# Optimization experiments

Measured on AMD Instinct MI355X. Metric: run time of the kernel, lower is better.

Reference implementation:

```python
import jax, jax.numpy as jnp
import numpy as np
from jax import lax

TEMPLATE = 21          # template_size
SEARCH = 9             # search_range
PAD = TEMPLATE // 2    # conv padding


def setup_inputs() -> dict:
    key = jax.random.key(0)
    k1, k2 = jax.random.split(key)
    B, H, W = 4, 480, 640
    p1 = jax.random.uniform(k1, (B, 1, H, W), dtype=jnp.float32)
    p2 = jax.random.uniform(k2, (B, 1, H, W), dtype=jnp.float32)
    return {"p1": p1, "p2": p2}


def _box_sum(x):
    # 21x21 box filter (conv with all-ones kernel), same padding, stride 1.
    kernel = jnp.ones((1, 1, TEMPLATE, TEMPLATE), x.dtype)
    return lax.conv_general_dilated(x, kernel, (1, 1), [(PAD, PAD), (PAD, PAD)])


def reference(p1, p2):
    p1 = p1.astype(jnp.float32)
    p2 = p2.astype(jnp.float32)
    B, _, H, W = p1.shape
    R = SEARCH

    # zero-pad search margin around p2
    p2_padded = jnp.pad(p2, ((0, 0), (0, 0), (R, R), (R, R)))

    # (361, 2) offsets, iterated dy-major / dx-minor to match the torch loop order
    dys, dxs = jnp.meshgrid(jnp.arange(-R, R + 1), jnp.arange(-R, R + 1), indexing='ij')
    offsets = jnp.stack([dys.reshape(-1), dxs.reshape(-1)], axis=-1)  # rows: (dy, dx)

    max0 = jnp.full((B, 1, H, W), -1.0, dtype=jnp.float32)
    flow0 = jnp.zeros((B, 2, H, W), dtype=jnp.float32)

    def step(carry, off):
        max_score, flow = carry
        dy, dx = off[0], off[1]
        shifted = lax.dynamic_slice(p2_padded, (0, 0, R + dy, R + dx), (B, 1, H, W))
        agreement = p1 * shifted + (1.0 - p1) * (1.0 - shifted)
        corr = _box_sum(agreement)                  # (B,1,H,W)
        mask = corr > max_score
        max_score = jnp.where(mask, corr, max_score)
        m = mask[:, 0]                               # (B,H,W)
        fx = jnp.where(m, dx.astype(jnp.float32), flow[:, 0])
        fy = jnp.where(m, dy.astype(jnp.float32), flow[:, 1])
        flow = jnp.stack([fx, fy], axis=1)
        return (max_score, flow), None

    (max_score, flow), _ = lax.scan(step, (max0, flow0), offsets)

    particle_density = _box_sum(p1)
    confidence = jnp.clip(particle_density / float(TEMPLATE * TEMPLATE), 0.0, 1.0)
    return flow, confidence
```

## Files before the change

### kernel.cpp

```cpp
#include <hip/hip_runtime.h>


#define HH 480
#define WW 640
#define TH 32
#define TW 32
#define QROWS 52
#define PROWS 70
#define PCOLS 70
#define PSTR  71
#define RSTR  36
#define MARGIN 0.002f
#define NPIX (4 * HH * WW)

__device__ __forceinline__ float replay_corr(const float* __restrict__ p1b,
                                             const float* __restrict__ p2b,
                                             int y, int x, int k) {
  int dy = k / 19 - 9, dx = k % 19 - 9;
  float s = 0.f;
  for (int u = 0; u < 21; ++u) {
    int yy = y - 10 + u;
    if (yy < 0 || yy >= HH) continue;
    int y2 = yy + dy;
    bool yok = (y2 >= 0 && y2 < HH);
    const float* r1 = p1b + yy * WW;
    const float* r2 = p2b + y2 * WW;
#pragma unroll
    for (int v = 0; v < 21; ++v) {
      int xx = x - 10 + v;
      if (xx < 0 || xx >= WW) continue;
      float p = r1[xx];
      int x2 = xx + dx;
      float s2 = (yok && x2 >= 0 && x2 < WW) ? r2[x2] : 0.f;
      float t2 = __fmul_rn(__fsub_rn(1.f, p), __fsub_rn(1.f, s2));
      float agr = __fmaf_rn(p, s2, t2);
      s = __fadd_rn(s, agr);
    }
  }
  return s;
}

__global__ __launch_bounds__(256, 4)
void bcm_pass1(const float* __restrict__ p1, const float* __restrict__ p2,
               float* __restrict__ out, unsigned* __restrict__ wl,
               unsigned capE) {
  __shared__ float ps[PROWS * PSTR];
  __shared__ __align__(16) float rsb0[QROWS * RSTR];
  __shared__ __align__(16) float rsb1[QROWS * RSTR];

  const int tid = threadIdx.x;
  const int b  = blockIdx.z;
  const int y0 = blockIdx.y * TH;
  const int x0 = blockIdx.x * TW;
  const float* p1b = p1 + b * HH * WW;
  const float* p2b = p2 + b * HH * WW;

  for (int i = tid; i < PROWS * PCOLS; i += 256) {
    int rr = i / PCOLS, cc = i - rr * PCOLS;
    int Y = y0 - 19 + rr, X = x0 - 19 + cc;
    float v = 0.f;
    if (Y >= 0 && Y < HH && X >= 0 && X < WW) v = p2b[Y * WW + X];
    ps[rr * PSTR + cc] = v;
  }

  const int col = tid & 31;
  const int r0  = (tid >> 5) * 4;
  const int prow_ = tid >> 2;
  const int c0    = (tid & 3) * 8;
  const bool active1 = (prow_ < QROWS);

  float qreg[28];
  if (active1) {
    int Y = y0 - 10 + prow_;
    bool yok = (Y >= 0 && Y < HH);
    const float* qrow = p1b + Y * WW;
#pragma unroll
    for (int t = 0; t < 28; ++t) {
      int X = x0 - 10 + c0 + t;
      float v = 0.f;
      if (yok && X >= 0 && X < WW) v = 2.f * qrow[X] - 1.f;
      qreg[t] = v;
    }
  }
  __syncthreads();

  float bv[4][4];
  int   bk[4][4];
#pragma unroll
  for (int j = 0; j < 4; ++j)
#pragma unroll
    for (int t = 0; t < 4; ++t) { bv[j][t] = -1e30f; bk[j][t] = 0; }

  float preg[28];
  int k = 0;
  for (int dy = -9; dy <= 9; ++dy) {
    const float* prowp = active1 ? &ps[(prow_ + dy + 9) * PSTR + c0] : ps;
    if (active1) {
#pragma unroll
      for (int t = 0; t < 28; ++t) preg[t] = prowp[t];
    }
#pragma unroll
    for (int dxi = 0; dxi < 19; ++dxi, ++k) {
      float* slab = (k & 1) ? rsb1 : rsb0;
      if (active1) {
        float s = 0.f;
#pragma unroll
        for (int t = 0; t < 21; ++t) s += qreg[t] * preg[(dxi + t) % 28];
        float rs[8];
        rs[0] = s;
#pragma unroll
        for (int j = 1; j < 8; ++j) {
          s += qreg[j + 20] * preg[(dxi + j + 20) % 28]
             - qreg[j - 1] * preg[(dxi + j - 1) % 28];
          rs[j] = s;
        }
        float4* w = (float4*)&slab[prow_ * RSTR + c0];
        w[0] = make_float4(rs[0], rs[1], rs[2], rs[3]);
        w[1] = make_float4(rs[4], rs[5], rs[6], rs[7]);
        if (dxi < 18) preg[dxi % 28] = prowp[dxi + 28];
      }
      __syncthreads();
      {
        float s = 0.f;
#pragma unroll
        for (int u = 0; u < 21; ++u) s += slab[(r0 + u) * RSTR + col];
#pragma unroll
        for (int j = 0; j < 4; ++j) {
          if (j > 0) s += slab[(r0 + 20 + j) * RSTR + col]
                        - slab[(r0 + j - 1) * RSTR + col];
          float cv = s;
          if (cv > bv[j][3]) {
            int ck = k;
#pragma unroll
            for (int t = 0; t < 4; ++t) {
              if (cv > bv[j][t]) {
                float tv = bv[j][t]; int tk = bk[j][t];
                bv[j][t] = cv; bk[j][t] = ck;
                cv = tv; ck = tk;
              }
            }
          }
        }
      }
    }
  }

  __syncthreads();
  if (active1) {
    float s = 0.f;
#pragma unroll
    for (int t = 0; t < 21; ++t) s += qreg[t];
    float rs[8];
    rs[0] = s;
#pragma unroll
    for (int j = 1; j < 8; ++j) {
      s += qreg[j + 20] - qreg[j - 1];
      rs[j] = s;
    }
    float4* w = (float4*)&rsb0[prow_ * RSTR + c0];
    w[0] = make_float4(rs[0], rs[1], rs[2], rs[3]);
    w[1] = make_float4(rs[4], rs[5], rs[6], rs[7]);
  }
  __syncthreads();

  unsigned* cntN = wl;
  unsigned* cntD = wl + 1;
  uint4* entries = (uint4*)(wl + 8);
  const unsigned capHalf = capE >> 1;
  const int confoff = 4 * 2 * HH * WW;
  {
    float s = 0.f;
#pragma unroll
    for (int u = 0; u < 21; ++u) s += rsb0[(r0 + u) * RSTR + col];
#pragma unroll
    for (int j = 0; j < 4; ++j) {
      if (j > 0) s += rsb0[(r0 + 20 + j) * RSTR + col]
                    - rsb0[(r0 + j - 1) * RSTR + col];
      int y = y0 + r0 + j;
      int x = x0 + col;
      int ny = min(y + 10, HH - 1) - max(y - 10, 0) + 1;
      int nx = min(x + 10, WW - 1) - max(x - 10, 0) + 1;
      float c = (s + (float)(ny * nx)) * (1.f / 882.f);
      float conf = fminf(fmaxf(c, 0.f), 1.f);

      int kwin = bk[j][0];
      float ofx = (float)(kwin % 19 - 9);
      float ofy = (float)(kwin / 19 - 9);

      if (bv[j][0] - bv[j][1] <= MARGIN) {
        int cand[4];
        int n = 1; cand[0] = bk[j][0];
#pragma unroll
        for (int t = 1; t < 4; ++t)
          if (bv[j][0] - bv[j][t] <= MARGIN) cand[n++] = bk[j][t];
        bool deep = (bv[j][0] - bv[j][3] <= MARGIN);
        unsigned pix = (unsigned)((b * HH + y) * WW + x);
        bool stored = false;
        if (!deep) {
          unsigned slot = atomicAdd(cntN, 1u);
          if (slot < capHalf) {
            unsigned kk[4];
#pragma unroll
            for (int t = 0; t < 4; ++t)
              kk[t] = (t < n) ? (unsigned)cand[t] : 0xFFFFu;
            uint4 e;
            e.x = pix;
            e.y = kk[0] | (kk[1] << 16);
            e.z = kk[2] | (kk[3] << 16);
            e.w = 0u;
            entries[slot] = e;
            stored = true;
          }
        } else {
          unsigned ds = atomicAdd(cntD, 1u);
          if (ds < capHalf) {
            uint4 e; e.x = pix; e.y = 0u; e.z = 0u; e.w = 0u;
            entries[capE - 1 - ds] = e;
            stored = true;
          }
        }
        if (!stored) {
          int c2 = (n > 2) ? cand[2] : cand[0];
          int c3 = (n > 3) ? cand[3] : cand[0];
          int dpf = deep ? 1 : 0;
          ofx = (float)(1000000 + cand[0] + 512 * cand[1]);
          ofy = (float)(c2 + 512 * c3 + 262144 * dpf);
        }
      }
      out[((b * 2 + 0) * HH + y) * WW + x] = ofx;
      out[((b * 2 + 1) * HH + y) * WW + x] = ofy;
      out[confoff + (b * HH + y) * WW + x] = conf;
    }
  }
}

__global__ __launch_bounds__(256)
void bcm_pass2(const float* __restrict__ p1, const float* __restrict__ p2,
               float* __restrict__ out, const unsigned* __restrict__ wl,
               unsigned capE) {
  const unsigned capHalf = capE >> 1;
  unsigned rawN = wl[0], rawD = wl[1];
  unsigned nN = rawN > capHalf ? capHalf : rawN;
  unsigned nD = rawD > capHalf ? capHalf : rawD;
  const uint4* entries = (const uint4*)(wl + 8);
  const int lane = threadIdx.x & 63;
  unsigned wid = blockIdx.x * (blockDim.x >> 6) + (threadIdx.x >> 6);
  unsigned nw = gridDim.x * (blockDim.x >> 6);

  for (unsigned base = wid * 16; base < nN; base += nw * 16) {
    unsigned e = base + (lane >> 2);
    int c = lane & 3;
    float wv = -1e30f;
    int   wk = 0x7FFF;
    unsigned pix = 0;
    bool valid = (e < nN);
    if (valid) {
      uint4 ent = entries[e];
      pix = ent.x;
      unsigned kc = (c == 0) ? (ent.y & 0xFFFFu) :
                    (c == 1) ? (ent.y >> 16) :
                    (c == 2) ? (ent.z & 0xFFFFu) : (ent.z >> 16);
      if (kc != 0xFFFFu) {
        int b = pix / (HH * WW);
        int r = pix - b * (HH * WW);
        int y = r / WW, x = r - y * WW;
        wv = replay_corr(p1 + b * HH * WW, p2 + b * HH * WW, y, x, (int)kc);
        wk = (int)kc;
      }
    }
#pragma unroll
    for (int d = 1; d <= 2; d <<= 1) {
      float ov = __shfl_xor(wv, d, 64);
      int   ok = __shfl_xor(wk, d, 64);
      if (ov > wv || (ov == wv && ok < wk)) { wv = ov; wk = ok; }
    }
    if (valid && c == 0) {
      int b = pix / (HH * WW);
      int r = pix - b * (HH * WW);
      int y = r / WW, x = r - y * WW;
      int fxi = (b * 2 * HH + y) * WW + x;
      out[fxi] = (float)(wk % 19 - 9);
      out[fxi + HH * WW] = (float)(wk / 19 - 9);
    }
  }

  for (unsigned d = wid; d < nD; d += nw) {
    uint4 ent = entries[capE - 1 - d];
    unsigned pix = ent.x;
    int b = pix / (HH * WW);
    int r = pix - b * (HH * WW);
    int y = r / WW, x = r - y * WW;
    const float* p1b = p1 + b * HH * WW;
    const float* p2b = p2 + b * HH * WW;
    float wv = -1e30f;
    int   wk = 0x7FFF;
    for (int k = lane; k < 361; k += 64) {
      float s = replay_corr(p1b, p2b, y, x, k);
      if (s > wv || (s == wv && k < wk)) { wv = s; wk = k; }
    }
    for (int off = 32; off > 0; off >>= 1) {
      float ov = __shfl_down(wv, off, 64);
      int   ok = __shfl_down(wk, off, 64);
      if (ov > wv || (ov == wv && ok < wk)) { wv = ov; wk = ok; }
    }
    if (lane == 0) {
      int fxi = (b * 2 * HH + y) * WW + x;
      out[fxi] = (float)(wk % 19 - 9);
      out[fxi + HH * WW] = (float)(wk / 19 - 9);
    }
  }

  if (rawN > capHalf || rawD > capHalf) {
    int stride = gridDim.x * blockDim.x;
    for (int idx = blockIdx.x * blockDim.x + threadIdx.x; idx < NPIX;
         idx += stride) {
      int b = idx / (HH * WW);
      int r = idx - b * (HH * WW);
      int fxi = b * 2 * HH * WW + r;
      float fx = out[fxi];
      if (fx < 500000.f) continue;
      int fyi = fxi + HH * WW;
      int p = (int)fx - 1000000;
      int q = (int)out[fyi];
      int deep = q >> 18;
      int kk[4] = {p & 511, p >> 9, q & 511, (q >> 9) & 511};
      int y = r / WW, x = r - y * WW;
      const float* p1b = p1 + b * HH * WW;
      const float* p2b = p2 + b * HH * WW;
      float wv = 0.f; int win = -1;
      if (deep) {
        for (int k = 0; k < 361; ++k) {
          float s = replay_corr(p1b, p2b, y, x, k);
          if (win < 0 || s > wv) { wv = s; win = k; }
        }
      } else {
        for (int c = 0; c < 4; ++c) {
          int k = kk[c];
          float s = replay_corr(p1b, p2b, y, x, k);
          if (win < 0 || s > wv || (s == wv && k < win)) { wv = s; win = k; }
        }
      }
      out[fxi] = (float)(win % 19 - 9);
      out[fyi] = (float)(win / 19 - 9);
    }
  }
}

extern "C" void kernel_launch(void* const* d_in, const int* in_sizes, int n_in,
                              void* d_out, int out_size, void* d_ws, size_t ws_size,
                              hipStream_t stream) {
  const float* p1 = (const float*)d_in[0];
  const float* p2 = (const float*)d_in[1];
  float* out = (float*)d_out;
  unsigned* wl = (unsigned*)d_ws;
  unsigned capE = (ws_size >= 64) ? (unsigned)((ws_size - 32) / 16) : 0u;
  hipMemsetAsync(d_ws, 0, 32, stream);
  dim3 grid1(WW / TW, HH / TH, 4);
  bcm_pass1<<<grid1, dim3(256), 0, stream>>>(p1, p2, out, wl, capE);
  bcm_pass2<<<dim3(512), dim3(256), 0, stream>>>(p1, p2, out, wl, capE);
}
```

Baseline: 720.7 us.

## Split FMA reduction chains into independent accumulators and wave-parallelize overflow replay

The row-sum and column-sum reductions in the main correlation loop now use four independent accumulators and precomputed sliding deltas instead of one serial dependency chain, aiming for more instruction-level parallelism. Column loads are hoisted into a register array. The overflow fallback path, which replayed correlations one pixel per thread, now ballots flagged pixels within each wave and replays each one cooperatively across the 64 lanes through a shared helper. Reassociating the float sums can change rounding, which risks flipping near-tie argmax decisions and adds register pressure.

```diff
diff --git a/kernel.cpp b/kernel.cpp
--- a/kernel.cpp
+++ b/kernel.cpp
@@ -40,6 +40,41 @@
   return s;
 }
 
+__device__ __forceinline__ void replay_reduce_write(
+    const float* p1, const float* p2, float* out,
+    unsigned pix, bool deep, unsigned k0, unsigned k1, unsigned k2,
+    unsigned k3, int lane) {
+  int b = pix / (HH * WW);
+  int r = pix - b * (HH * WW);
+  int y = r / WW, x = r - y * WW;
+  const float* p1b = p1 + b * HH * WW;
+  const float* p2b = p2 + b * HH * WW;
+  float wv = -1e30f;
+  int   wk = 0x7FFF;
+  if (deep) {
+    for (int k = lane; k < 361; k += 64) {
+      float s = replay_corr(p1b, p2b, y, x, k);
+      if (s > wv || (s == wv && k < wk)) { wv = s; wk = k; }
+    }
+  } else if (lane < 4) {
+    unsigned kc = (lane == 0) ? k0 : (lane == 1) ? k1 : (lane == 2) ? k2 : k3;
+    if (kc != 0xFFFFu) {
+      wv = replay_corr(p1b, p2b, y, x, (int)kc);
+      wk = (int)kc;
+    }
+  }
+  for (int off = 32; off > 0; off >>= 1) {
+    float ov = __shfl_down(wv, off, 64);
+    int   ok = __shfl_down(wk, off, 64);
+    if (ov > wv || (ov == wv && ok < wk)) { wv = ov; wk = ok; }
+  }
+  if (lane == 0) {
+    int fxi = (b * 2 * HH + y) * WW + x;
+    out[fxi] = (float)(wk % 19 - 9);
+    out[fxi + HH * WW] = (float)(wk / 19 - 9);
+  }
+}
+
 __global__ __launch_bounds__(256, 4)
 void bcm_pass1(const float* __restrict__ p1, const float* __restrict__ p2,
                float* __restrict__ out, unsigned* __restrict__ wl,
@@ -103,17 +138,25 @@
     for (int dxi = 0; dxi < 19; ++dxi, ++k) {
       float* slab = (k & 1) ? rsb1 : rsb0;
       if (active1) {
-        float s = 0.f;
-#pragma unroll
-        for (int t = 0; t < 21; ++t) s += qreg[t] * preg[(dxi + t) % 28];
+        float a0 = 0.f, a1 = 0.f, a2 = 0.f, a3 = 0.f;
+#pragma unroll
+        for (int t = 0; t < 20; t += 4) {
+          a0 += qreg[t]     * preg[(dxi + t)     % 28];
+          a1 += qreg[t + 1] * preg[(dxi + t + 1) % 28];
+          a2 += qreg[t + 2] * preg[(dxi + t + 2) % 28];
+          a3 += qreg[t + 3] * preg[(dxi + t + 3) % 28];
+        }
+        a0 += qreg[20] * preg[(dxi + 20) % 28];
+        float s = (a0 + a1) + (a2 + a3);
+        float d[7];
+#pragma unroll
+        for (int j = 1; j < 8; ++j)
+          d[j - 1] = qreg[j + 20] * preg[(dxi + j + 20) % 28]
+                   - qreg[j - 1] * preg[(dxi + j - 1) % 28];
         float rs[8];
         rs[0] = s;
 #pragma unroll
-        for (int j = 1; j < 8; ++j) {
-          s += qreg[j + 20] * preg[(dxi + j + 20) % 28]
-             - qreg[j - 1] * preg[(dxi + j - 1) % 28];
-          rs[j] = s;
-        }
+        for (int j = 1; j < 8; ++j) rs[j] = rs[j - 1] + d[j - 1];
         float4* w = (float4*)&slab[prow_ * RSTR + c0];
         w[0] = make_float4(rs[0], rs[1], rs[2], rs[3]);
         w[1] = make_float4(rs[4], rs[5], rs[6], rs[7]);
@@ -121,14 +164,24 @@
       }
       __syncthreads();
       {
-        float s = 0.f;
-#pragma unroll
-        for (int u = 0; u < 21; ++u) s += slab[(r0 + u) * RSTR + col];
+        float v[24];
+#pragma unroll
+        for (int u = 0; u < 24; ++u) v[u] = slab[(r0 + u) * RSTR + col];
+        float a0 = 0.f, a1 = 0.f, a2 = 0.f, a3 = 0.f;
+#pragma unroll
+        for (int u = 0; u < 20; u += 4) {
+          a0 += v[u]; a1 += v[u + 1]; a2 += v[u + 2]; a3 += v[u + 3];
+        }
+        a0 += v[20];
+        float s = (a0 + a1) + (a2 + a3);
+        float ws[4];
+        ws[0] = s;
+        ws[1] = ws[0] + (v[21] - v[0]);
+        ws[2] = ws[1] + (v[22] - v[1]);
+        ws[3] = ws[2] + (v[23] - v[2]);
 #pragma unroll
         for (int j = 0; j < 4; ++j) {
-          if (j > 0) s += slab[(r0 + 20 + j) * RSTR + col]
-                        - slab[(r0 + j - 1) * RSTR + col];
-          float cv = s;
+          float cv = ws[j];
           if (cv > bv[j][3]) {
             int ck = k;
 #pragma unroll
@@ -286,62 +339,34 @@
 
   for (unsigned d = wid; d < nD; d += nw) {
     uint4 ent = entries[capE - 1 - d];
-    unsigned pix = ent.x;
-    int b = pix / (HH * WW);
-    int r = pix - b * (HH * WW);
-    int y = r / WW, x = r - y * WW;
-    const float* p1b = p1 + b * HH * WW;
-    const float* p2b = p2 + b * HH * WW;
-    float wv = -1e30f;
-    int   wk = 0x7FFF;
-    for (int k = lane; k < 361; k += 64) {
-      float s = replay_corr(p1b, p2b, y, x, k);
-      if (s > wv || (s == wv && k < wk)) { wv = s; wk = k; }
-    }
-    for (int off = 32; off > 0; off >>= 1) {
-      float ov = __shfl_down(wv, off, 64);
-      int   ok = __shfl_down(wk, off, 64);
-      if (ov > wv || (ov == wv && ok < wk)) { wv = ov; wk = ok; }
-    }
-    if (lane == 0) {
-      int fxi = (b * 2 * HH + y) * WW + x;
-      out[fxi] = (float)(wk % 19 - 9);
-      out[fxi + HH * WW] = (float)(wk / 19 - 9);
-    }
+    replay_reduce_write(p1, p2, out, ent.x, true, 0, 0, 0, 0, lane);
   }
 
   if (rawN > capHalf || rawD > capHalf) {
-    int stride = gridDim.x * blockDim.x;
-    for (int idx = blockIdx.x * blockDim.x + threadIdx.x; idx < NPIX;
-         idx += stride) {
-      int b = idx / (HH * WW);
-      int r = idx - b * (HH * WW);
-      int fxi = b * 2 * HH * WW + r;
-      float fx = out[fxi];
-      if (fx < 500000.f) continue;
-      int fyi = fxi + HH * WW;
-      int p = (int)fx - 1000000;
-      int q = (int)out[fyi];
-      int deep = q >> 18;
-      int kk[4] = {p & 511, p >> 9, q & 511, (q >> 9) & 511};
-      int y = r / WW, x = r - y * WW;
-      const float* p1b = p1 + b * HH * WW;
-      const float* p2b = p2 + b * HH * WW;
-      float wv = 0.f; int win = -1;
-      if (deep) {
-        for (int k = 0; k < 361; ++k) {
-          float s = replay_corr(p1b, p2b, y, x, k);
-          if (win < 0 || s > wv) { wv = s; win = k; }
-        }
-      } else {
-        for (int c = 0; c < 4; ++c) {
-          int k = kk[c];
-          float s = replay_corr(p1b, p2b, y, x, k);
-          if (win < 0 || s > wv || (s == wv && k < win)) { wv = s; win = k; }
-        }
-      }
-      out[fxi] = (float)(win % 19 - 9);
-      out[fyi] = (float)(win / 19 - 9);
+    for (unsigned base = wid * 64u; base < (unsigned)NPIX; base += nw * 64u) {
+      unsigned idx = base + lane;
+      float fx = 0.f;
+      if (idx < (unsigned)NPIX) {
+        int b = idx / (HH * WW);
+        int r = idx - b * (HH * WW);
+        fx = out[b * 2 * HH * WW + r];
+      }
+      unsigned long long m = __ballot(fx >= 500000.f);
+      while (m) {
+        int l = __ffsll((long long)m) - 1;
+        m &= m - 1;
+        unsigned sidx = base + (unsigned)l;
+        int b = sidx / (HH * WW);
+        int r = sidx - b * (HH * WW);
+        int fxi = b * 2 * HH * WW + r;
+        int p = (int)out[fxi] - 1000000;
+        int q = (int)out[fxi + HH * WW];
+        bool deep = (q >> 18) != 0;
+        unsigned k0 = (unsigned)(p & 511), k1 = (unsigned)(p >> 9);
+        unsigned k2 = (unsigned)(q & 511), k3 = (unsigned)((q >> 9) & 511);
+        replay_reduce_write(p1, p2, out, (unsigned)((b * HH) * WW) + r, deep,
+                            k0, k1, k2, k3, lane);
+      }
     }
   }
 }
```

Result: slower. 756.7 us (+5.0%).
